# Kernel tuning notes

Hardware: AMD Instinct MI355X
Metric: run time of the kernel (lower is better)

Reference implementation:

```python
import jax, jax.numpy as jnp
import numpy as np

N_NODES = 100000
IN_CH, HID_CH, OUT_CH = 128, 64, 8
N_EDGES = 3200000


def gcn_conv(x, src, dst, W, b, n):
    # PyG GCNConv: linear transform, add self-loops, symmetric deg^-1/2
    # normalization, scatter-add aggregation at target nodes, then bias.
    h = x @ W                                   # [N, out]
    loop = jnp.arange(n)
    s = jnp.concatenate([src, loop])            # [E+N]
    d = jnp.concatenate([dst, loop])
    deg = jax.ops.segment_sum(jnp.ones_like(d, h.dtype), d, num_segments=n)
    dinv = jnp.where(deg > 0, jax.lax.rsqrt(deg), 0.0)
    norm = dinv[s] * dinv[d]                    # [E+N]
    msgs = norm[:, None] * h[s]                 # gather + scale, [E+N, out]
    out = jax.ops.segment_sum(msgs, d, num_segments=n)  # scatter-add
    return out + b


def setup_inputs() -> dict:
    key = jax.random.key(0)
    k1, k2, k3, k4, k5, k6 = jax.random.split(key, 6)
    x = jax.random.normal(k1, (N_NODES, IN_CH), dtype=jnp.float32)
    edge_index = jax.random.randint(k2, (2, N_EDGES), 0, N_NODES, dtype=jnp.int64)
    # Glorot-style init for the two GCNConv layers
    W1 = jax.random.normal(k3, (IN_CH, HID_CH), dtype=jnp.float32) / np.sqrt(IN_CH)
    b1 = jnp.zeros((HID_CH,), dtype=jnp.float32)
    W2 = jax.random.normal(k4, (HID_CH, OUT_CH), dtype=jnp.float32) / np.sqrt(HID_CH)
    b2 = jnp.zeros((OUT_CH,), dtype=jnp.float32)
    return {"x": x, "edge_index": edge_index, "W1": W1, "b1": b1, "W2": W2, "b2": b2}


def reference(x, edge_index, W1, b1, W2, b2):
    n = x.shape[0]
    src, dst = edge_index[0], edge_index[1]
    h = gcn_conv(x, src, dst, W1, b1, n)
    h = jax.nn.relu(h)
    h = gcn_conv(h, src, dst, W2, b2, n)
    return jax.nn.log_softmax(h, axis=1)
```

## Files before the change

### kernel.cpp

```cpp
#include <hip/hip_runtime.h>
#include <hip/hip_fp16.h>
#include <hip/hip_fp8.h>

#define IN_CH  128
#define HID_CH 64
#define OUT_CH 8
#define BSH    8
#define BCAP   8960
#define PCHUNK 8192
#define LDK    136

typedef unsigned long long ull;
typedef float floatx2 __attribute__((ext_vector_type(2)));
typedef _Float16 f16x8 __attribute__((ext_vector_type(8)));
typedef float f32x4 __attribute__((ext_vector_type(4)));


__device__ __forceinline__ unsigned char f2fp8(float f) {
    __hip_fp8_e4m3 t(f);
    return (unsigned char)t.__x;
}
__device__ __forceinline__ float fp82f(unsigned char b) {
    __hip_fp8_e4m3 t;
    t.__x = (__hip_fp8_storage_t)b;
    return (float)t;
}

__device__ __forceinline__ void acc8(float* acc, ull p) {
#if __has_builtin(__builtin_amdgcn_cvt_pk_f32_fp8)
    unsigned lo = (unsigned)p, hi = (unsigned)(p >> 32);
    floatx2 q0 = __builtin_amdgcn_cvt_pk_f32_fp8(lo, false);
    floatx2 q1 = __builtin_amdgcn_cvt_pk_f32_fp8(lo, true);
    floatx2 q2 = __builtin_amdgcn_cvt_pk_f32_fp8(hi, false);
    floatx2 q3 = __builtin_amdgcn_cvt_pk_f32_fp8(hi, true);
    acc[0] += q0.x; acc[1] += q0.y; acc[2] += q1.x; acc[3] += q1.y;
    acc[4] += q2.x; acc[5] += q2.y; acc[6] += q3.x; acc[7] += q3.y;
#else
#pragma unroll
    for (int j = 0; j < 8; ++j) acc[j] += fp82f((unsigned char)(p >> (8 * j)));
#endif
}

__global__ __launch_bounds__(512) void part_k(const int* __restrict__ ei, int E, int NB,
                                              int* __restrict__ gcnt,
                                              unsigned* __restrict__ bucket) {
    __shared__ int cnt[512];
    __shared__ int scn[512];
    __shared__ int gbase[512];
    __shared__ unsigned ordered[PCHUNK];
    int t = threadIdx.x;
    int c0 = blockIdx.x * PCHUNK;
    const int* __restrict__ src = ei;
    const int* __restrict__ dst = ei + E;

    cnt[t] = 0;
    __syncthreads();
    for (int i = t; i < PCHUNK; i += 512) {
        int e = c0 + i;
        if (e < E) atomicAdd(&cnt[dst[e] >> BSH], 1);
    }
    __syncthreads();
    scn[t] = cnt[t];
    __syncthreads();
    for (int o = 1; o < 512; o <<= 1) {
        int v = (t >= o) ? scn[t - o] : 0;
        __syncthreads();
        scn[t] += v;
        __syncthreads();
    }
    int ex = scn[t] - cnt[t];
    __syncthreads();
    scn[t] = ex;
    int cn = cnt[t];
    gbase[t] = (t < NB && cn > 0) ? atomicAdd(&gcnt[t], cn) : 0;
    __syncthreads();
    cnt[t] = 0;
    __syncthreads();
    for (int i = t; i < PCHUNK; i += 512) {
        int e = c0 + i;
        if (e < E) {
            int s = src[e], d = dst[e];
            int k = d >> BSH;
            int slot = scn[k] + atomicAdd(&cnt[k], 1);
            ordered[slot] = (unsigned)s | ((unsigned)(d & 255) << 24);
        }
    }
    __syncthreads();
    int tot = scn[511] + cnt[511];
    for (int i = t; i < tot; i += 512) {
        int lo = 0, hi = 512;
        #pragma unroll
        for (int it = 0; it < 10; ++it) {
            int mid = (lo + hi) >> 1;
            if (scn[mid] > i) hi = mid; else lo = mid + 1;
        }
        int k = lo - 1;
        bucket[(size_t)k * BCAP + gbase[k] + (i - scn[k])] = ordered[i];
    }
}

__global__ __launch_bounds__(256) void sort_k(unsigned* __restrict__ bucket,
                                              const int* __restrict__ gcnt,
                                              int* __restrict__ deg,
                                              float* __restrict__ dinv,
                                              int* __restrict__ off, int n) {
    __shared__ int cnt[256];
    __shared__ int excl[256];
    __shared__ int cur[256];
    __shared__ int ordered[BCAP];
    int bk = blockIdx.x;
    int t = threadIdx.x;
    int node0 = bk << BSH;
    cnt[t] = 0;
    __syncthreads();
    int ecnt = gcnt[bk];
    unsigned* __restrict__ bb = bucket + (size_t)bk * BCAP;
    for (int i = t; i < ecnt; i += 256) {
        unsigned p = bb[i];
        atomicAdd(&cnt[p >> 24], 1);
    }
    __syncthreads();
    int dg = cnt[t];
    excl[t] = dg;
    __syncthreads();
    for (int o = 1; o < 256; o <<= 1) {
        int v = (t >= o) ? excl[t - o] : 0;
        __syncthreads();
        excl[t] += v;
        __syncthreads();
    }
    int ex = excl[t] - dg;
    __syncthreads();
    excl[t] = ex;
    cur[t] = 0;
    int node = node0 + t;
    if (node < n) {
        deg[node]  = dg;
        dinv[node] = rsqrtf((float)dg + 1.0f);
        off[node]  = bk * BCAP + ex;
    }
    __syncthreads();
    for (int i = t; i < ecnt; i += 256) {
        unsigned p = bb[i];
        int s = (int)(p & 0xFFFFFFu), d = (int)(p >> 24);
        int slot = excl[d] + atomicAdd(&cur[d], 1);
        ordered[slot] = s;
    }
    __syncthreads();
    int* __restrict__ csr = (int*)bb;
    for (int i = t; i < ecnt; i += 256) csr[i] = ordered[i];
}

__global__ __launch_bounds__(256) void gemm1_k(const float* __restrict__ x,
                                               const float* __restrict__ W,
                                               const float* __restrict__ dinv,
                                               unsigned char* __restrict__ h, int n) {
    __shared__ __align__(16) float uShared[64 * 68];
    __shared__ __align__(16) _Float16 Wt[64 * LDK];
    int t = threadIdx.x;
    int node0 = blockIdx.x * 64;
    _Float16* xs = (_Float16*)uShared;

    for (int i = t; i < 64 * 32; i += 256) {
        int row = i >> 5, c4 = i & 31;
        int node = node0 + row;
        float4 v = (node < n) ? *(const float4*)(x + (size_t)node * IN_CH + c4 * 4)
                              : make_float4(0.f, 0.f, 0.f, 0.f);
        _Float16* dstp = xs + row * LDK + c4 * 4;
        dstp[0] = (_Float16)v.x; dstp[1] = (_Float16)v.y;
        dstp[2] = (_Float16)v.z; dstp[3] = (_Float16)v.w;
    }
    for (int i = t; i < IN_CH * HID_CH; i += 256) {
        int k = i >> 6, nn = i & 63;
        Wt[nn * LDK + k] = (_Float16)W[i];
    }
    __syncthreads();

    int w = t >> 6, lane = t & 63;
    int rsel = lane & 15, ksel = lane >> 4;
    f32x4 acc[4];
#pragma unroll
    for (int ct = 0; ct < 4; ++ct) acc[ct] = (f32x4){0.f, 0.f, 0.f, 0.f};

#pragma unroll
    for (int kk = 0; kk < 4; ++kk) {
        f16x8 a = *(const f16x8*)(xs + (16 * w + rsel) * LDK + kk * 32 + ksel * 8);
#pragma unroll
        for (int ct = 0; ct < 4; ++ct) {
            f16x8 b = *(const f16x8*)(Wt + (ct * 16 + rsel) * LDK + kk * 32 + ksel * 8);
            acc[ct] = __builtin_amdgcn_mfma_f32_16x16x32_f16(a, b, acc[ct], 0, 0, 0);
        }
    }
    __syncthreads();
    float* outS = uShared;
#pragma unroll
    for (int ct = 0; ct < 4; ++ct)
#pragma unroll
        for (int r = 0; r < 4; ++r)
            outS[(16 * w + ksel * 4 + r) * 68 + ct * 16 + rsel] = acc[ct][r];
    __syncthreads();

    {
        int row = t >> 2, quad = t & 3;
        int node = node0 + row;
        if (node < n) {
            float dv = dinv[node];
            const float* srcp = outS + row * 68 + quad * 16;
            unsigned un[4];
#pragma unroll
            for (int g = 0; g < 4; ++g) {
                unsigned v = 0;
#pragma unroll
                for (int j = 0; j < 4; ++j)
                    v |= (unsigned)f2fp8(srcp[g * 4 + j] * dv) << (8 * j);
                un[g] = v;
            }
            *(uint4*)(h + (size_t)node * HID_CH + quad * 16) = make_uint4(un[0], un[1], un[2], un[3]);
        }
    }
}

__global__ __launch_bounds__(256) void agg1_gather_k(const int* __restrict__ off,
                                                     const int* __restrict__ deg,
                                                     const int* __restrict__ csr,
                                                     const float* __restrict__ dinv,
                                                     const unsigned char* __restrict__ h,
                                                     const float* __restrict__ b1,
                                                     __half* __restrict__ z, int n) {
    int tid = threadIdx.x;
    int node = blockIdx.x * 4 + (tid >> 6);
    if (node >= n) return;
    int lane = tid & 63;
    int e8 = lane >> 3, cg = lane & 7;

    float acc[8];
#pragma unroll
    for (int j = 0; j < 8; ++j) acc[j] = 0.0f;

    if (e8 == 0)
        acc8(acc, *(const ull*)(h + (size_t)node * HID_CH + cg * 8));

    int o = off[node], end = o + deg[node];
    int i = o + e8;
    for (; i + 24 < end; i += 32) {
        int s0 = csr[i], s1 = csr[i + 8], s2 = csr[i + 16], s3 = csr[i + 24];
        ull p0 = *(const ull*)(h + (size_t)s0 * HID_CH + cg * 8);
        ull p1 = *(const ull*)(h + (size_t)s1 * HID_CH + cg * 8);
        ull p2 = *(const ull*)(h + (size_t)s2 * HID_CH + cg * 8);
        ull p3 = *(const ull*)(h + (size_t)s3 * HID_CH + cg * 8);
        acc8(acc, p0); acc8(acc, p1); acc8(acc, p2); acc8(acc, p3);
    }
    for (; i < end; i += 8)
        acc8(acc, *(const ull*)(h + (size_t)csr[i] * HID_CH + cg * 8));

#pragma unroll
    for (int j = 0; j < 8; ++j) {
        acc[j] += __shfl_xor(acc[j], 8);
        acc[j] += __shfl_xor(acc[j], 16);
        acc[j] += __shfl_xor(acc[j], 32);
    }

    if (e8 == 0) {
        float dv = dinv[node];
        union { __half2 hv[4]; uint4 u; } pk;
#pragma unroll
        for (int j2 = 0; j2 < 4; ++j2) {
            float z0 = fmaxf(dv * acc[2 * j2]      + b1[cg * 8 + 2 * j2],     0.0f);
            float z1v = fmaxf(dv * acc[2 * j2 + 1] + b1[cg * 8 + 2 * j2 + 1], 0.0f);
            pk.hv[j2] = __floats2half2_rn(z0, z1v);
        }
        *(uint4*)(z + (size_t)node * HID_CH + cg * 8) = pk.u;
    }
}

__global__ __launch_bounds__(256) void gemm2_k(const __half* __restrict__ z,
                                               const float* __restrict__ W,
                                               const float* __restrict__ dinv,
                                               __half* __restrict__ h2, int n) {
    __shared__ float Ws[HID_CH * OUT_CH];
    int tid = threadIdx.x;
    for (int i = tid; i < HID_CH * OUT_CH; i += 256) Ws[i] = W[i];
    __syncthreads();
    int node = blockIdx.x * 256 + tid;
    if (node >= n) return;
    float acc[OUT_CH];
#pragma unroll
    for (int c = 0; c < OUT_CH; ++c) acc[c] = 0.0f;
    const __half2* zr = (const __half2*)(z + (size_t)node * HID_CH);
#pragma unroll 8
    for (int k2 = 0; k2 < HID_CH / 2; ++k2) {
        float2 v = __half22float2(zr[k2]);
        int k = k2 * 2;
#pragma unroll
        for (int c = 0; c < OUT_CH; ++c)
            acc[c] += v.x * Ws[k * OUT_CH + c] + v.y * Ws[(k + 1) * OUT_CH + c];
    }
    float dv = dinv[node];
    __half2* o2 = (__half2*)(h2 + (size_t)node * OUT_CH);
#pragma unroll
    for (int c2 = 0; c2 < OUT_CH / 2; ++c2)
        o2[c2] = __floats2half2_rn(dv * acc[2 * c2], dv * acc[2 * c2 + 1]);
}

__global__ __launch_bounds__(256) void agg2_final_k(const int* __restrict__ off,
                                                    const int* __restrict__ deg,
                                                    const int* __restrict__ csr,
                                                    const float* __restrict__ dinv,
                                                    const __half* __restrict__ h2,
                                                    const float* __restrict__ b,
                                                    float* __restrict__ out, int n) {
    int tid = threadIdx.x;
    int node = blockIdx.x * 32 + (tid >> 3);
    int c = tid & 7;
    if (node >= n) return;
    float dv = dinv[node];
    int o = off[node], dg = deg[node];
    float a0 = 0, a1 = 0, a2 = 0, a3 = 0;
    int i = o, end = o + dg;
    for (; i + 3 < end; i += 4) {
        int s0 = csr[i], s1 = csr[i + 1], s2 = csr[i + 2], s3 = csr[i + 3];
        a0 += __half2float(h2[(size_t)s0 * OUT_CH + c]);
        a1 += __half2float(h2[(size_t)s1 * OUT_CH + c]);
        a2 += __half2float(h2[(size_t)s2 * OUT_CH + c]);
        a3 += __half2float(h2[(size_t)s3 * OUT_CH + c]);
    }
    for (; i < end; ++i) a0 += __half2float(h2[(size_t)csr[i] * OUT_CH + c]);
    float self = __half2float(h2[(size_t)node * OUT_CH + c]);
    float val = dv * ((a0 + a1) + (a2 + a3) + self) + b[c];
    float m = val;
    m = fmaxf(m, __shfl_xor(m, 1, 8));
    m = fmaxf(m, __shfl_xor(m, 2, 8));
    m = fmaxf(m, __shfl_xor(m, 4, 8));
    float s8 = expf(val - m);
    s8 += __shfl_xor(s8, 1, 8);
    s8 += __shfl_xor(s8, 2, 8);
    s8 += __shfl_xor(s8, 4, 8);
    out[(size_t)node * OUT_CH + c] = val - m - logf(s8);
}

extern "C" void kernel_launch(void* const* d_in, const int* in_sizes, int n_in,
                              void* d_out, int out_size, void* d_ws, size_t ws_size,
                              hipStream_t stream) {
    const float* x  = (const float*)d_in[0];
    const int*   ei = (const int*)d_in[1];
    const float* W1 = (const float*)d_in[2];
    const float* b1 = (const float*)d_in[3];
    const float* W2 = (const float*)d_in[4];
    const float* b2 = (const float*)d_in[5];
    float* out = (float*)d_out;

    const int n = in_sizes[0] / IN_CH;
    const int E = in_sizes[1] / 2;
    const int NP = 100352;
    const int NB = (n + 255) >> BSH;

    int*      deg    = (int*)d_ws;
    float*    dinv   = (float*)(deg + NP);
    int*      gcnt   = (int*)(dinv + NP);
    int*      off    = gcnt + 512;
    unsigned* bucket = (unsigned*)(off + NP);
    unsigned char* h1 = (unsigned char*)(bucket + (size_t)NB * BCAP);
    __half*   z1     = (__half*)(h1 + (size_t)NP * HID_CH);
    __half*   h2     = z1 + (size_t)NP * HID_CH;
    int*      csr    = (int*)bucket;

    const int NCH = (E + PCHUNK - 1) / PCHUNK;

    hipMemsetAsync(gcnt, 0, 512 * sizeof(int), stream);
    part_k<<<NCH, 512, 0, stream>>>(ei, E, NB, gcnt, bucket);
    sort_k<<<NB, 256, 0, stream>>>(bucket, gcnt, deg, dinv, off, n);
    gemm1_k<<<(n + 63) / 64, 256, 0, stream>>>(x, W1, dinv, h1, n);
    agg1_gather_k<<<(n + 3) / 4, 256, 0, stream>>>(off, deg, csr, dinv, h1, b1, z1, n);
    gemm2_k<<<(n + 255) / 256, 256, 0, stream>>>(z1, W2, dinv, h2, n);
    agg2_final_k<<<(n + 31) / 32, 256, 0, stream>>>(off, deg, csr, dinv, h2, b2, out, n);
}
```

Measured before the change: 166.2 us.

## Split layer-1 aggregation into two channel halves and drop partition binary search

Layer-1 hidden features are stored as two separate 32-channel fp8 arrays, and aggregation runs as two passes so each gather table is half the size and more likely to stay cache-resident. Each wave now covers 16 edges by 4 channel groups. The partition kernel also records each slot's bucket id in shared memory, so the scatter no longer needs a binary search. The cost is reading the CSR indices and offsets twice, one extra launch, and more shared memory in the partition kernel.

After: 194.5 us. 17.0% more time.

```diff
diff --git a/kernel.cpp b/kernel.cpp
--- a/kernel.cpp
+++ b/kernel.cpp
@@ -8,7 +8,6 @@
 #define BSH    8
 #define BCAP   8960
 #define PCHUNK 8192
-#define LDK    136
 
 typedef unsigned long long ull;
 typedef float floatx2 __attribute__((ext_vector_type(2)));
@@ -48,6 +47,7 @@
     __shared__ int scn[512];
     __shared__ int gbase[512];
     __shared__ unsigned ordered[PCHUNK];
+    __shared__ unsigned short ordK[PCHUNK];
     int t = threadIdx.x;
     int c0 = blockIdx.x * PCHUNK;
     const int* __restrict__ src = ei;
@@ -83,18 +83,13 @@
             int k = d >> BSH;
             int slot = scn[k] + atomicAdd(&cnt[k], 1);
             ordered[slot] = (unsigned)s | ((unsigned)(d & 255) << 24);
+            ordK[slot] = (unsigned short)k;
         }
     }
     __syncthreads();
     int tot = scn[511] + cnt[511];
     for (int i = t; i < tot; i += 512) {
-        int lo = 0, hi = 512;
-        #pragma unroll
-        for (int it = 0; it < 10; ++it) {
-            int mid = (lo + hi) >> 1;
-            if (scn[mid] > i) hi = mid; else lo = mid + 1;
-        }
-        int k = lo - 1;
+        int k = ordK[i];
         bucket[(size_t)k * BCAP + gbase[k] + (i - scn[k])] = ordered[i];
     }
 }
@@ -151,10 +146,12 @@
     for (int i = t; i < ecnt; i += 256) csr[i] = ordered[i];
 }
 
+#define LDK 136
 __global__ __launch_bounds__(256) void gemm1_k(const float* __restrict__ x,
                                                const float* __restrict__ W,
                                                const float* __restrict__ dinv,
-                                               unsigned char* __restrict__ h, int n) {
+                                               unsigned char* __restrict__ hlo,
+                                               unsigned char* __restrict__ hhi, int n) {
     __shared__ __align__(16) float uShared[64 * 68];
     __shared__ __align__(16) _Float16 Wt[64 * LDK];
     int t = threadIdx.x;
@@ -215,61 +212,65 @@
                     v |= (unsigned)f2fp8(srcp[g * 4 + j] * dv) << (8 * j);
                 un[g] = v;
             }
-            *(uint4*)(h + (size_t)node * HID_CH + quad * 16) = make_uint4(un[0], un[1], un[2], un[3]);
+            unsigned char* dstp = (quad < 2)
+                ? (hlo + (size_t)node * 32 + quad * 16)
+                : (hhi + (size_t)node * 32 + (quad - 2) * 16);
+            *(uint4*)dstp = make_uint4(un[0], un[1], un[2], un[3]);
         }
     }
 }
 
-__global__ __launch_bounds__(256) void agg1_gather_k(const int* __restrict__ off,
-                                                     const int* __restrict__ deg,
-                                                     const int* __restrict__ csr,
-                                                     const float* __restrict__ dinv,
-                                                     const unsigned char* __restrict__ h,
-                                                     const float* __restrict__ b1,
-                                                     __half* __restrict__ z, int n) {
+__global__ __launch_bounds__(256) void agg1_half_k(const int* __restrict__ off,
+                                                   const int* __restrict__ deg,
+                                                   const int* __restrict__ csr,
+                                                   const float* __restrict__ dinv,
+                                                   const unsigned char* __restrict__ h,
+                                                   const float* __restrict__ b1h,
+                                                   __half* __restrict__ zh, int n) {
     int tid = threadIdx.x;
     int node = blockIdx.x * 4 + (tid >> 6);
     if (node >= n) return;
     int lane = tid & 63;
-    int e8 = lane >> 3, cg = lane & 7;
+    int e16 = lane >> 2, cg = lane & 3;
 
     float acc[8];
 #pragma unroll
     for (int j = 0; j < 8; ++j) acc[j] = 0.0f;
 
-    if (e8 == 0)
-        acc8(acc, *(const ull*)(h + (size_t)node * HID_CH + cg * 8));
+    if (e16 == 0)
+        acc8(acc, *(const ull*)(h + (size_t)node * 32 + cg * 8));
 
     int o = off[node], end = o + deg[node];
-    int i = o + e8;
-    for (; i + 24 < end; i += 32) {
-        int s0 = csr[i], s1 = csr[i + 8], s2 = csr[i + 16], s3 = csr[i + 24];
-        ull p0 = *(const ull*)(h + (size_t)s0 * HID_CH + cg * 8);
-        ull p1 = *(const ull*)(h + (size_t)s1 * HID_CH + cg * 8);
-        ull p2 = *(const ull*)(h + (size_t)s2 * HID_CH + cg * 8);
-        ull p3 = *(const ull*)(h + (size_t)s3 * HID_CH + cg * 8);
+    int i = o + e16;
+    for (; i + 48 < end; i += 64) {
+        int s0 = csr[i], s1 = csr[i + 16], s2 = csr[i + 32], s3 = csr[i + 48];
+        ull p0 = *(const ull*)(h + (size_t)s0 * 32 + cg * 8);
+        ull p1 = *(const ull*)(h + (size_t)s1 * 32 + cg * 8);
+        ull p2 = *(const ull*)(h + (size_t)s2 * 32 + cg * 8);
+        ull p3 = *(const ull*)(h + (size_t)s3 * 32 + cg * 8);
         acc8(acc, p0); acc8(acc, p1); acc8(acc, p2); acc8(acc, p3);
     }
-    for (; i < end; i += 8)
-        acc8(acc, *(const ull*)(h + (size_t)csr[i] * HID_CH + cg * 8));
+    for (; i < end; i += 16)
+        acc8(acc, *(const ull*)(h + (size_t)csr[i] * 32 + cg * 8));
 
 #pragma unroll
     for (int j = 0; j < 8; ++j) {
+        acc[j] += __shfl_xor(acc[j], 4);
         acc[j] += __shfl_xor(acc[j], 8);
         acc[j] += __shfl_xor(acc[j], 16);
         acc[j] += __shfl_xor(acc[j], 32);
     }
 
-    if (e8 == 0) {
+    if (e16 == 0) {
         float dv = dinv[node];
         union { __half2 hv[4]; uint4 u; } pk;
 #pragma unroll
         for (int j2 = 0; j2 < 4; ++j2) {
-            float z0 = fmaxf(dv * acc[2 * j2]      + b1[cg * 8 + 2 * j2],     0.0f);
-            float z1v = fmaxf(dv * acc[2 * j2 + 1] + b1[cg * 8 + 2 * j2 + 1], 0.0f);
+            float z0 = fmaxf(dv * acc[2 * j2]      + b1h[cg * 8 + 2 * j2],     0.0f);
+            float z1v = fmaxf(dv * acc[2 * j2 + 1] + b1h[cg * 8 + 2 * j2 + 1], 0.0f);
             pk.hv[j2] = __floats2half2_rn(z0, z1v);
         }
-        *(uint4*)(z + (size_t)node * HID_CH + cg * 8) = pk.u;
+        *(uint4*)(zh + (size_t)node * HID_CH + cg * 8) = pk.u;
     }
 }
 
@@ -359,8 +360,9 @@
     int*      gcnt   = (int*)(dinv + NP);
     int*      off    = gcnt + 512;
     unsigned* bucket = (unsigned*)(off + NP);
-    unsigned char* h1 = (unsigned char*)(bucket + (size_t)NB * BCAP);
-    __half*   z1     = (__half*)(h1 + (size_t)NP * HID_CH);
+    unsigned char* h1lo = (unsigned char*)(bucket + (size_t)NB * BCAP);
+    unsigned char* h1hi = h1lo + (size_t)NP * 32;
+    __half*   z1     = (__half*)(h1hi + (size_t)NP * 32);
     __half*   h2     = z1 + (size_t)NP * HID_CH;
     int*      csr    = (int*)bucket;
 
@@ -369,8 +371,9 @@
     hipMemsetAsync(gcnt, 0, 512 * sizeof(int), stream);
     part_k<<<NCH, 512, 0, stream>>>(ei, E, NB, gcnt, bucket);
     sort_k<<<NB, 256, 0, stream>>>(bucket, gcnt, deg, dinv, off, n);
-    gemm1_k<<<(n + 63) / 64, 256, 0, stream>>>(x, W1, dinv, h1, n);
-    agg1_gather_k<<<(n + 3) / 4, 256, 0, stream>>>(off, deg, csr, dinv, h1, b1, z1, n);
+    gemm1_k<<<(n + 63) / 64, 256, 0, stream>>>(x, W1, dinv, h1lo, h1hi, n);
+    agg1_half_k<<<(n + 3) / 4, 256, 0, stream>>>(off, deg, csr, dinv, h1lo, b1,      z1,      n);
+    agg1_half_k<<<(n + 3) / 4, 256, 0, stream>>>(off, deg, csr, dinv, h1hi, b1 + 32, z1 + 32, n);
     gemm2_k<<<(n + 255) / 256, 256, 0, stream>>>(z1, W2, dinv, h2, n);
     agg2_final_k<<<(n + 31) / 32, 256, 0, stream>>>(off, deg, csr, dinv, h2, b2, out, n);
 }
```

## Fuse layer-2 GEMM into layer-1 aggregation and store bucket ids in partition

Applied to the files above, without the earlier changes.

The second linear transform (64->8), together with bias and ReLU, now runs inside the layer-1 aggregation kernel. Each wavefront computes its node's 8 outputs through a per-lane partial dot product and a shuffle reduction, so the fp16 z1 intermediate is never written or re-read and one launch is removed. Separately, the partition kernel records each edge's bucket index in shared memory, which replaces the 10-step binary search in the scatter loop with a lookup. The trade-off is 16 KB of extra LDS per partition block and an extra W2 load at the start of every aggregation block.

After: 170.8 us. +2.8%, slower.

```diff
diff --git a/kernel.cpp b/kernel.cpp
--- a/kernel.cpp
+++ b/kernel.cpp
@@ -8,7 +8,6 @@
 #define BSH    8
 #define BCAP   8960
 #define PCHUNK 8192
-#define LDK    136
 
 typedef unsigned long long ull;
 typedef float floatx2 __attribute__((ext_vector_type(2)));
@@ -48,6 +47,7 @@
     __shared__ int scn[512];
     __shared__ int gbase[512];
     __shared__ unsigned ordered[PCHUNK];
+    __shared__ unsigned short ordK[PCHUNK];
     int t = threadIdx.x;
     int c0 = blockIdx.x * PCHUNK;
     const int* __restrict__ src = ei;
@@ -83,18 +83,13 @@
             int k = d >> BSH;
             int slot = scn[k] + atomicAdd(&cnt[k], 1);
             ordered[slot] = (unsigned)s | ((unsigned)(d & 255) << 24);
+            ordK[slot] = (unsigned short)k;
         }
     }
     __syncthreads();
     int tot = scn[511] + cnt[511];
     for (int i = t; i < tot; i += 512) {
-        int lo = 0, hi = 512;
-        #pragma unroll
-        for (int it = 0; it < 10; ++it) {
-            int mid = (lo + hi) >> 1;
-            if (scn[mid] > i) hi = mid; else lo = mid + 1;
-        }
-        int k = lo - 1;
+        int k = ordK[i];
         bucket[(size_t)k * BCAP + gbase[k] + (i - scn[k])] = ordered[i];
     }
 }
@@ -151,6 +146,7 @@
     for (int i = t; i < ecnt; i += 256) csr[i] = ordered[i];
 }
 
+#define LDK 136
 __global__ __launch_bounds__(256) void gemm1_k(const float* __restrict__ x,
                                                const float* __restrict__ W,
                                                const float* __restrict__ dinv,
@@ -220,14 +216,21 @@
     }
 }
 
-__global__ __launch_bounds__(256) void agg1_gather_k(const int* __restrict__ off,
-                                                     const int* __restrict__ deg,
-                                                     const int* __restrict__ csr,
-                                                     const float* __restrict__ dinv,
-                                                     const unsigned char* __restrict__ h,
-                                                     const float* __restrict__ b1,
-                                                     __half* __restrict__ z, int n) {
+__global__ __launch_bounds__(256) void agg1_fused_k(const int* __restrict__ off,
+                                                    const int* __restrict__ deg,
+                                                    const int* __restrict__ csr,
+                                                    const float* __restrict__ dinv,
+                                                    const unsigned char* __restrict__ h,
+                                                    const float* __restrict__ b1,
+                                                    const float* __restrict__ W2,
+                                                    __half* __restrict__ h2, int n) {
+    __shared__ float W2s[HID_CH * OUT_CH];
+    __shared__ float b1s[HID_CH];
     int tid = threadIdx.x;
+    for (int i = tid; i < HID_CH * OUT_CH; i += 256) W2s[i] = W2[i];
+    if (tid < HID_CH) b1s[tid] = b1[tid];
+    __syncthreads();
+
     int node = blockIdx.x * 4 + (tid >> 6);
     if (node >= n) return;
     int lane = tid & 63;
@@ -260,46 +263,19 @@
         acc[j] += __shfl_xor(acc[j], 32);
     }
 
-    if (e8 == 0) {
-        float dv = dinv[node];
-        union { __half2 hv[4]; uint4 u; } pk;
-#pragma unroll
-        for (int j2 = 0; j2 < 4; ++j2) {
-            float z0 = fmaxf(dv * acc[2 * j2]      + b1[cg * 8 + 2 * j2],     0.0f);
-            float z1v = fmaxf(dv * acc[2 * j2 + 1] + b1[cg * 8 + 2 * j2 + 1], 0.0f);
-            pk.hv[j2] = __floats2half2_rn(z0, z1v);
-        }
-        *(uint4*)(z + (size_t)node * HID_CH + cg * 8) = pk.u;
-    }
-}
-
-__global__ __launch_bounds__(256) void gemm2_k(const __half* __restrict__ z,
-                                               const float* __restrict__ W,
-                                               const float* __restrict__ dinv,
-                                               __half* __restrict__ h2, int n) {
-    __shared__ float Ws[HID_CH * OUT_CH];
-    int tid = threadIdx.x;
-    for (int i = tid; i < HID_CH * OUT_CH; i += 256) Ws[i] = W[i];
-    __syncthreads();
-    int node = blockIdx.x * 256 + tid;
-    if (node >= n) return;
-    float acc[OUT_CH];
-#pragma unroll
-    for (int c = 0; c < OUT_CH; ++c) acc[c] = 0.0f;
-    const __half2* zr = (const __half2*)(z + (size_t)node * HID_CH);
-#pragma unroll 8
-    for (int k2 = 0; k2 < HID_CH / 2; ++k2) {
-        float2 v = __half22float2(zr[k2]);
-        int k = k2 * 2;
-#pragma unroll
-        for (int c = 0; c < OUT_CH; ++c)
-            acc[c] += v.x * Ws[k * OUT_CH + c] + v.y * Ws[(k + 1) * OUT_CH + c];
-    }
     float dv = dinv[node];
-    __half2* o2 = (__half2*)(h2 + (size_t)node * OUT_CH);
-#pragma unroll
-    for (int c2 = 0; c2 < OUT_CH / 2; ++c2)
-        o2[c2] = __floats2half2_rn(dv * acc[2 * c2], dv * acc[2 * c2 + 1]);
+    float pc = 0.0f;
+#pragma unroll
+    for (int j = 0; j < 8; ++j) {
+        float zj = fmaxf(dv * acc[j] + b1s[cg * 8 + j], 0.0f);
+        pc += zj * W2s[(cg * 8 + j) * OUT_CH + e8];
+    }
+    pc += __shfl_xor(pc, 1);
+    pc += __shfl_xor(pc, 2);
+    pc += __shfl_xor(pc, 4);
+
+    if (cg == 0)
+        h2[(size_t)node * OUT_CH + e8] = __float2half(dv * pc);
 }
 
 __global__ __launch_bounds__(256) void agg2_final_k(const int* __restrict__ off,
@@ -360,8 +336,7 @@
     int*      off    = gcnt + 512;
     unsigned* bucket = (unsigned*)(off + NP);
     unsigned char* h1 = (unsigned char*)(bucket + (size_t)NB * BCAP);
-    __half*   z1     = (__half*)(h1 + (size_t)NP * HID_CH);
-    __half*   h2     = z1 + (size_t)NP * HID_CH;
+    __half*   h2     = (__half*)(h1 + (size_t)NP * HID_CH);
     int*      csr    = (int*)bucket;
 
     const int NCH = (E + PCHUNK - 1) / PCHUNK;
@@ -370,7 +345,6 @@
     part_k<<<NCH, 512, 0, stream>>>(ei, E, NB, gcnt, bucket);
     sort_k<<<NB, 256, 0, stream>>>(bucket, gcnt, deg, dinv, off, n);
     gemm1_k<<<(n + 63) / 64, 256, 0, stream>>>(x, W1, dinv, h1, n);
-    agg1_gather_k<<<(n + 3) / 4, 256, 0, stream>>>(off, deg, csr, dinv, h1, b1, z1, n);
-    gemm2_k<<<(n + 255) / 256, 256, 0, stream>>>(z1, W2, dinv, h2, n);
+    agg1_fused_k<<<(n + 3) / 4, 256, 0, stream>>>(off, deg, csr, dinv, h1, b1, W2, h2, n);
     agg2_final_k<<<(n + 31) / 32, 256, 0, stream>>>(off, deg, csr, dinv, h2, b2, out, n);
 }
```
